# Optimization experiments

Measured on AMD Instinct MI355X. Metric: run time of the kernel, lower is better.

Reference implementation:

```python
import jax, jax.numpy as jnp
import numpy as np

N_NODES = 200000  # graph size
D = 128           # feature dim == out_size
N1 = 81920        # layer-1 node set size
B = 8192          # batch size
K = 10            # num_sample neighbors


def setup_inputs() -> dict:
    key = jax.random.key(0)
    k = jax.random.split(key, 7)
    raw_features = jax.random.normal(k[0], (N_NODES, D), dtype=jnp.float32)
    # xavier-like scale for weights [out, 2*in]
    W1 = jax.random.normal(k[1], (D, 2 * D), dtype=jnp.float32) * (1.0 / np.sqrt(2 * D))
    W2 = jax.random.normal(k[2], (D, 2 * D), dtype=jnp.float32) * (1.0 / np.sqrt(2 * D))
    layer1_nodes = jax.random.randint(k[3], (N1,), 0, N_NODES)
    neigh0_idx = jax.random.randint(k[4], (N1, K), 0, N_NODES)
    map_batch = jax.random.randint(k[5], (B,), 0, N1)
    neigh1_idx = jax.random.randint(k[6], (B, K), 0, N1)
    return {
        "raw_features": raw_features,
        "W1": W1,
        "W2": W2,
        "layer1_nodes": layer1_nodes,
        "neigh0_idx": neigh0_idx,
        "map_batch": map_batch,
        "neigh1_idx": neigh1_idx,
    }


def _sage_layer(self_feats, agg_feats, W):
    # combined = cat([self, agg], dim=1); relu(W @ combined.T).T == relu(combined @ W.T)
    combined = jnp.concatenate([self_feats, agg_feats], axis=1)
    return jax.nn.relu(combined @ W.T)


def reference(raw_features, W1, W2, layer1_nodes, neigh0_idx, map_batch, neigh1_idx):
    # Layer 1: aggregate raw features over K sampled neighbors (MEAN), gcn=False
    agg0 = jnp.mean(raw_features[neigh0_idx], axis=1)        # [N1, D]
    self0 = raw_features[layer1_nodes]                        # [N1, D]
    h1 = _sage_layer(self0, agg0, W1)                         # [N1, D]
    # Layer 2: aggregate layer-1 embeddings for the batch nodes
    agg1 = jnp.mean(h1[neigh1_idx], axis=1)                   # [B, D]
    self1 = h1[map_batch]                                     # [B, D]
    h2 = _sage_layer(self1, agg1, W2)                         # [B, D]
    return h2
```

## Files before the change

### kernel.cpp

```cpp
#include <hip/hip_runtime.h>
#include <stdint.h>

#define D 128
#define K_NEI 10
#define TILE_M 64

typedef __bf16 bf16x8 __attribute__((ext_vector_type(8)));
typedef float f32x4 __attribute__((ext_vector_type(4)));

__device__ __forceinline__ uint32_t f2bf(float f) {
    union { float f; uint32_t u; } v; v.f = f;
    uint32_t u = v.u;
    return (u + 0x7FFFu + ((u >> 16) & 1u)) >> 16;
}
__device__ __forceinline__ float bf2f(uint32_t h) {
    union { uint32_t u; float f; } v; v.u = h << 16; return v.f;
}
__device__ __forceinline__ uint32_t pack2(float a, float b) {
    return f2bf(a) | (f2bf(b) << 16);
}

__global__ void convert_W(const float* __restrict__ W, uint16_t* __restrict__ Wb)
{
    int t = blockIdx.x * 256 + threadIdx.x;
    int c = t >> 4, j = t & 15;
    const float* src = W + (size_t)(c & 127) * 256 + (c >> 7) * 128 + j * 8;
    f32x4 a = *(const f32x4*)src;
    f32x4 b = *(const f32x4*)(src + 4);
    uint4 o;
    o.x = pack2(a[0], a[1]); o.y = pack2(a[2], a[3]);
    o.z = pack2(b[0], b[1]); o.w = pack2(b[2], b[3]);
    *(uint4*)(Wb + (size_t)c * 128 + j * 8) = o;
}

template <bool A_F32>
__global__ void gemm_P(const void* __restrict__ Asrc_,
                       const uint16_t* __restrict__ Wb,
                       uint16_t* __restrict__ P)
{
    __shared__ __align__(16) uint16_t Alds[TILE_M * 128];
    __shared__ __align__(16) uint16_t Wlds[128 * 128];

    const int tid  = threadIdx.x;
    const int wave = tid >> 6;
    const int lane = tid & 63;
    const int r16  = lane & 15;
    const int q    = lane >> 4;
    const int G    = blockIdx.x * TILE_M;

    #pragma unroll
    for (int it = 0; it < 4; ++it) {
        int t = it * 256 + tid;
        int n = t >> 4, c = t & 15;
        uint4 o;
        if (A_F32) {
            const float* src = (const float*)Asrc_ + (size_t)(G + n) * D + c * 8;
            f32x4 a = *(const f32x4*)src;
            f32x4 b = *(const f32x4*)(src + 4);
            o.x = pack2(a[0], a[1]); o.y = pack2(a[2], a[3]);
            o.z = pack2(b[0], b[1]); o.w = pack2(b[2], b[3]);
        } else {
            o = *(const uint4*)((const uint16_t*)Asrc_ + (size_t)(G + n) * D + c * 8);
        }
        int cs = c ^ (n & 15);
        *(uint4*)(Alds + n * 128 + cs * 8) = o;
    }

    f32x4 acc[2][8];
    #pragma unroll
    for (int h = 0; h < 2; ++h)
        #pragma unroll
        for (int nt = 0; nt < 8; ++nt) acc[h][nt] = (f32x4){0.f, 0.f, 0.f, 0.f};

    for (int h = 0; h < 2; ++h) {
        #pragma unroll
        for (int it = 0; it < 8; ++it) {
            int t = it * 256 + tid;
            int j = t >> 4, c = t & 15;
            uint4 v = *(const uint4*)(Wb + (size_t)(h * 128 + j) * 128 + c * 8);
            int cs = c ^ (j & 15);
            *(uint4*)(Wlds + j * 128 + cs * 8) = v;
        }
        __syncthreads();

        #pragma unroll
        for (int ks = 0; ks < 4; ++ks) {
            int cidx = ks * 4 + q;
            bf16x8 a = *(const bf16x8*)(Alds + (wave * 16 + r16) * 128 + ((cidx ^ r16) * 8));
            bf16x8 b[8];
            #pragma unroll
            for (int nt = 0; nt < 8; ++nt) {
                int jj = nt * 16 + r16;
                b[nt] = *(const bf16x8*)(Wlds + jj * 128 + ((cidx ^ r16) * 8));
            }
            #pragma unroll
            for (int nt = 0; nt < 8; ++nt)
                acc[h][nt] = __builtin_amdgcn_mfma_f32_16x16x32_bf16(a, b[nt], acc[h][nt], 0, 0, 0);
        }
        __syncthreads();
    }

    const int row_base = G + wave * 16 + q * 4;
    #pragma unroll
    for (int h = 0; h < 2; ++h)
        #pragma unroll
        for (int nt = 0; nt < 8; ++nt) {
            int col = h * 128 + nt * 16 + r16;
            #pragma unroll
            for (int r = 0; r < 4; ++r)
                P[(size_t)(row_base + r) * 256 + col] = (uint16_t)f2bf(acc[h][nt][r]);
        }
}

template <bool OUT_F32>
__global__ void combine(const uint16_t* __restrict__ P,
                        const int* __restrict__ self_idx,
                        const int* __restrict__ neigh_idx,
                        void* __restrict__ out_, int M)
{
    const int t = blockIdx.x * 256 + threadIdx.x;
    const int i = t >> 4;
    const int j = t & 15;
    if (i >= M) return;

    uint4 sv = *(const uint4*)(P + (size_t)self_idx[i] * 256 + j * 8);

    const int* nrow = neigh_idx + (size_t)i * K_NEI;
    int idx[K_NEI];
    #pragma unroll
    for (int k = 0; k < K_NEI; ++k) idx[k] = nrow[k];

    float s0=0,s1=0,s2=0,s3=0,s4=0,s5=0,s6=0,s7=0;
    #pragma unroll
    for (int k = 0; k < K_NEI; ++k) {
        uint4 v = *(const uint4*)(P + (size_t)idx[k] * 256 + 128 + j * 8);
        s0 += bf2f(v.x & 0xFFFFu); s1 += bf2f(v.x >> 16);
        s2 += bf2f(v.y & 0xFFFFu); s3 += bf2f(v.y >> 16);
        s4 += bf2f(v.z & 0xFFFFu); s5 += bf2f(v.z >> 16);
        s6 += bf2f(v.w & 0xFFFFu); s7 += bf2f(v.w >> 16);
    }
    const float inv = 0.1f;
    float r0 = bf2f(sv.x & 0xFFFFu) + s0 * inv, r1 = bf2f(sv.x >> 16) + s1 * inv;
    float r2 = bf2f(sv.y & 0xFFFFu) + s2 * inv, r3 = bf2f(sv.y >> 16) + s3 * inv;
    float r4 = bf2f(sv.z & 0xFFFFu) + s4 * inv, r5 = bf2f(sv.z >> 16) + s5 * inv;
    float r6 = bf2f(sv.w & 0xFFFFu) + s6 * inv, r7 = bf2f(sv.w >> 16) + s7 * inv;
    r0 = r0 > 0.f ? r0 : 0.f; r1 = r1 > 0.f ? r1 : 0.f;
    r2 = r2 > 0.f ? r2 : 0.f; r3 = r3 > 0.f ? r3 : 0.f;
    r4 = r4 > 0.f ? r4 : 0.f; r5 = r5 > 0.f ? r5 : 0.f;
    r6 = r6 > 0.f ? r6 : 0.f; r7 = r7 > 0.f ? r7 : 0.f;

    if (OUT_F32) {
        float* dst = (float*)out_ + (size_t)i * D + j * 8;
        *(f32x4*)dst       = (f32x4){r0, r1, r2, r3};
        *(f32x4*)(dst + 4) = (f32x4){r4, r5, r6, r7};
    } else {
        uint4 o;
        o.x = pack2(r0, r1); o.y = pack2(r2, r3);
        o.z = pack2(r4, r5); o.w = pack2(r6, r7);
        *(uint4*)((uint16_t*)out_ + (size_t)i * D + j * 8) = o;
    }
}

template <bool FEATS_F32>
__global__ void build_A(const void* __restrict__ feats_,
                        const int* __restrict__ self_idx,
                        const int* __restrict__ neigh_idx,
                        uint16_t* __restrict__ A, int M)
{
    const int t = blockIdx.x * 256 + threadIdx.x;
    const int i = t >> 4;
    const int j = t & 15;
    if (i >= M) return;

    const float*    ff = (const float*)feats_;
    const uint16_t* fb = (const uint16_t*)feats_;

    {
        int node = self_idx[i];
        uint4 o;
        if (FEATS_F32) {
            const float* src = ff + (size_t)node * D + j * 8;
            f32x4 a = *(const f32x4*)src;
            f32x4 b = *(const f32x4*)(src + 4);
            o.x = pack2(a[0], a[1]); o.y = pack2(a[2], a[3]);
            o.z = pack2(b[0], b[1]); o.w = pack2(b[2], b[3]);
        } else {
            o = *(const uint4*)(fb + (size_t)node * D + j * 8);
        }
        *(uint4*)(A + (size_t)i * 256 + j * 8) = o;
    }

    const int* nrow = neigh_idx + (size_t)i * K_NEI;
    int idx[K_NEI];
    #pragma unroll
    for (int k = 0; k < K_NEI; ++k) idx[k] = nrow[k];

    float s0=0,s1=0,s2=0,s3=0,s4=0,s5=0,s6=0,s7=0;
    #pragma unroll
    for (int k = 0; k < K_NEI; ++k) {
        if (FEATS_F32) {
            const float* src = ff + (size_t)idx[k] * D + j * 8;
            f32x4 a = *(const f32x4*)src;
            f32x4 b = *(const f32x4*)(src + 4);
            s0 += a[0]; s1 += a[1]; s2 += a[2]; s3 += a[3];
            s4 += b[0]; s5 += b[1]; s6 += b[2]; s7 += b[3];
        } else {
            uint4 v = *(const uint4*)(fb + (size_t)idx[k] * D + j * 8);
            s0 += bf2f(v.x & 0xFFFFu); s1 += bf2f(v.x >> 16);
            s2 += bf2f(v.y & 0xFFFFu); s3 += bf2f(v.y >> 16);
            s4 += bf2f(v.z & 0xFFFFu); s5 += bf2f(v.z >> 16);
            s6 += bf2f(v.w & 0xFFFFu); s7 += bf2f(v.w >> 16);
        }
    }
    const float inv = 0.1f;
    uint4 o;
    o.x = pack2(s0 * inv, s1 * inv);
    o.y = pack2(s2 * inv, s3 * inv);
    o.z = pack2(s4 * inv, s5 * inv);
    o.w = pack2(s6 * inv, s7 * inv);
    *(uint4*)(A + (size_t)i * 256 + 128 + j * 8) = o;
}

template <bool OUT_F32>
__global__ void gemm_relu(const uint16_t* __restrict__ A,
                          const float* __restrict__ W,
                          void* __restrict__ out_)
{
    __shared__ __align__(16) uint16_t Alds[TILE_M * 128];
    __shared__ __align__(16) uint16_t Wlds[128 * 128];

    const int tid  = threadIdx.x;
    const int wave = tid >> 6;
    const int lane = tid & 63;
    const int r16  = lane & 15;
    const int q    = lane >> 4;
    const int G    = blockIdx.x * TILE_M;

    f32x4 acc[8];
    #pragma unroll
    for (int nt = 0; nt < 8; ++nt) acc[nt] = (f32x4){0.f, 0.f, 0.f, 0.f};

    for (int half = 0; half < 2; ++half) {
        #pragma unroll
        for (int it = 0; it < 8; ++it) {
            int t = it * 256 + tid;
            int j = t >> 4, c = t & 15;
            const float* src = W + (size_t)j * 256 + half * 128 + c * 8;
            f32x4 w0 = *(const f32x4*)(src);
            f32x4 w1 = *(const f32x4*)(src + 4);
            uint4 o;
            o.x = pack2(w0[0], w0[1]); o.y = pack2(w0[2], w0[3]);
            o.z = pack2(w1[0], w1[1]); o.w = pack2(w1[2], w1[3]);
            int cs = c ^ (j & 15);
            *(uint4*)(Wlds + j * 128 + cs * 8) = o;
        }
        #pragma unroll
        for (int it = 0; it < 4; ++it) {
            int t = it * 256 + tid;
            int n = t >> 4, c = t & 15;
            uint4 v = *(const uint4*)(A + (size_t)(G + n) * 256 + half * 128 + c * 8);
            int cs = c ^ (n & 15);
            *(uint4*)(Alds + n * 128 + cs * 8) = v;
        }
        __syncthreads();

        #pragma unroll
        for (int ks = 0; ks < 4; ++ks) {
            int cidx = ks * 4 + q;
            bf16x8 a = *(const bf16x8*)(Alds + (wave * 16 + r16) * 128 + ((cidx ^ r16) * 8));
            bf16x8 b[8];
            #pragma unroll
            for (int nt = 0; nt < 8; ++nt) {
                int jj = nt * 16 + r16;
                b[nt] = *(const bf16x8*)(Wlds + jj * 128 + ((cidx ^ r16) * 8));
            }
            #pragma unroll
            for (int nt = 0; nt < 8; ++nt)
                acc[nt] = __builtin_amdgcn_mfma_f32_16x16x32_bf16(a, b[nt], acc[nt], 0, 0, 0);
        }
        __syncthreads();
    }

    const int row_base = G + wave * 16 + q * 4;
    #pragma unroll
    for (int nt = 0; nt < 8; ++nt) {
        int col = nt * 16 + r16;
        #pragma unroll
        for (int r = 0; r < 4; ++r) {
            float v = acc[nt][r];
            v = v > 0.f ? v : 0.f;
            if (OUT_F32) ((float*)out_)[(size_t)(row_base + r) * D + col] = v;
            else ((uint16_t*)out_)[(size_t)(row_base + r) * D + col] = (uint16_t)f2bf(v);
        }
    }
}

extern "C" void kernel_launch(void* const* d_in, const int* in_sizes, int n_in,
                              void* d_out, int out_size, void* d_ws, size_t ws_size,
                              hipStream_t stream) {
    const float* raw = (const float*)d_in[0];
    const float* W1  = (const float*)d_in[1];
    const float* W2  = (const float*)d_in[2];
    const int* layer1_nodes = (const int*)d_in[3];
    const int* neigh0       = (const int*)d_in[4];
    const int* map_batch    = (const int*)d_in[5];
    const int* neigh1       = (const int*)d_in[6];

    const int N_NODES = in_sizes[0] / D;
    const int N1 = in_sizes[3];
    const int B  = in_sizes[5];

    const size_t szP  = (size_t)N_NODES * 256 * 2;
    const size_t szQ  = (size_t)N1 * 256 * 2;
    const size_t szH1 = (size_t)N1 * 128 * 2;
    const size_t szW  = 256 * 128 * 2;
    const size_t needA = (szP > szQ ? szP : szQ) + szH1 + 2 * szW;

    if (ws_size >= needA && (N_NODES % TILE_M) == 0 && (N1 % TILE_M) == 0) {
        uint16_t* Pbuf = (uint16_t*)d_ws;
        uint16_t* h1   = (uint16_t*)((char*)d_ws + (szP > szQ ? szP : szQ));
        uint16_t* W1b  = h1 + (size_t)N1 * 128;
        uint16_t* W2b  = W1b + 256 * 128;

        convert_W<<<16, 256, 0, stream>>>(W1, W1b);
        convert_W<<<16, 256, 0, stream>>>(W2, W2b);
        gemm_P<true ><<<N_NODES / TILE_M, 256, 0, stream>>>(raw, W1b, Pbuf);
        combine<false><<<(N1 * 16 + 255) / 256, 256, 0, stream>>>(Pbuf, layer1_nodes, neigh0, h1, N1);
        gemm_P<false><<<N1 / TILE_M, 256, 0, stream>>>(h1, W2b, Pbuf);
        combine<true ><<<(B * 16 + 255) / 256, 256, 0, stream>>>(Pbuf, map_batch, neigh1, d_out, B);
        return;
    }

    const size_t needB = (size_t)N1 * 256 * 2 + (size_t)N1 * 128 * 2 + (size_t)B * 256 * 2;
    if (ws_size >= needB) {
        uint16_t* A1 = (uint16_t*)d_ws;
        uint16_t* h1 = A1 + (size_t)N1 * 256;
        uint16_t* A2 = h1 + (size_t)N1 * 128;

        build_A<true ><<<(N1 * 16 + 255) / 256, 256, 0, stream>>>(raw, layer1_nodes, neigh0, A1, N1);
        gemm_relu<false><<<N1 / TILE_M, 256, 0, stream>>>(A1, W1, h1);
        build_A<false><<<(B * 16 + 255) / 256, 256, 0, stream>>>(h1, map_batch, neigh1, A2, B);
        gemm_relu<true ><<<B / TILE_M, 256, 0, stream>>>(A2, W2, d_out);
    }
}
```

Before: 244.6 us.

## Make projection GEMM persistent with resident weights and register prefetch

The per-tile projection GEMM becomes a persistent kernel. It loads the full 256x128 bf16 weight matrix into shared memory once per block, then has each wave loop over 16-row tiles, reading A straight into registers and prefetching the next tile. This removes the repeated weight staging and the A shared-memory round trip that happened for every 64-row tile. The two weight conversions are merged into one launch, and neighbor indices are loaded as int2. The fallback path is replaced by a fused gather+GEMM layer kernel. The trade-off is 64KB of shared memory per block, which lowers occupancy.

```diff
diff --git a/kernel.cpp b/kernel.cpp
--- a/kernel.cpp
+++ b/kernel.cpp
@@ -19,10 +19,16 @@
 __device__ __forceinline__ uint32_t pack2(float a, float b) {
     return f2bf(a) | (f2bf(b) << 16);
 }
-
-__global__ void convert_W(const float* __restrict__ W, uint16_t* __restrict__ Wb)
+__device__ __forceinline__ bf16x8 u4_as_bf16x8(uint4 u) {
+    union { uint4 u; bf16x8 b; } v; v.u = u; return v.b;
+}
+
+__global__ void convert_W2(const float* __restrict__ Wa, const float* __restrict__ Wb_in,
+                           uint16_t* __restrict__ Oa, uint16_t* __restrict__ Ob)
 {
-    int t = blockIdx.x * 256 + threadIdx.x;
+    const float* W = (blockIdx.x < 16) ? Wa : Wb_in;
+    uint16_t*    O = (blockIdx.x < 16) ? Oa : Ob;
+    int t = (blockIdx.x & 15) * 256 + threadIdx.x;
     int c = t >> 4, j = t & 15;
     const float* src = W + (size_t)(c & 127) * 256 + (c >> 7) * 128 + j * 8;
     f32x4 a = *(const f32x4*)src;
@@ -30,86 +36,121 @@
     uint4 o;
     o.x = pack2(a[0], a[1]); o.y = pack2(a[2], a[3]);
     o.z = pack2(b[0], b[1]); o.w = pack2(b[2], b[3]);
-    *(uint4*)(Wb + (size_t)c * 128 + j * 8) = o;
+    *(uint4*)(O + (size_t)c * 128 + j * 8) = o;
 }
 
 template <bool A_F32>
-__global__ void gemm_P(const void* __restrict__ Asrc_,
-                       const uint16_t* __restrict__ Wb,
-                       uint16_t* __restrict__ P)
+__global__ __launch_bounds__(256)
+void gemm_ws(const void* __restrict__ Asrc_,
+             const uint16_t* __restrict__ Wb,
+             uint16_t* __restrict__ P, int M)
 {
-    __shared__ __align__(16) uint16_t Alds[TILE_M * 128];
-    __shared__ __align__(16) uint16_t Wlds[128 * 128];
+    __shared__ __align__(16) uint16_t Wlds[256 * 128];
 
     const int tid  = threadIdx.x;
     const int wave = tid >> 6;
     const int lane = tid & 63;
     const int r16  = lane & 15;
     const int q    = lane >> 4;
-    const int G    = blockIdx.x * TILE_M;
-
-    #pragma unroll
-    for (int it = 0; it < 4; ++it) {
+
+    #pragma unroll
+    for (int it = 0; it < 16; ++it) {
         int t = it * 256 + tid;
-        int n = t >> 4, c = t & 15;
-        uint4 o;
+        int j = t >> 4, c = t & 15;
+        uint4 v = *(const uint4*)(Wb + (size_t)j * 128 + c * 8);
+        int cs = c ^ (j & 15);
+        *(uint4*)(Wlds + j * 128 + cs * 8) = v;
+    }
+    __syncthreads();
+
+    const int nTiles = M >> 4;
+    const int stride = gridDim.x * 4;
+    int tile = blockIdx.x * 4 + wave;
+    if (tile >= nTiles) return;
+
+    f32x4 preF[8];  uint4 preB[4];
+
+    if (A_F32) {
+        const float* row = (const float*)Asrc_ + (size_t)(tile * 16 + r16) * D + q * 8;
+        #pragma unroll
+        for (int ks = 0; ks < 4; ++ks) {
+            preF[2 * ks]     = *(const f32x4*)(row + ks * 32);
+            preF[2 * ks + 1] = *(const f32x4*)(row + ks * 32 + 4);
+        }
+    } else {
+        const uint16_t* row = (const uint16_t*)Asrc_ + (size_t)(tile * 16 + r16) * D + q * 8;
+        #pragma unroll
+        for (int ks = 0; ks < 4; ++ks)
+            preB[ks] = *(const uint4*)(row + ks * 32);
+    }
+
+    while (tile < nTiles) {
+        const int nxt = tile + stride;
+
+        bf16x8 a[4];
         if (A_F32) {
-            const float* src = (const float*)Asrc_ + (size_t)(G + n) * D + c * 8;
-            f32x4 a = *(const f32x4*)src;
-            f32x4 b = *(const f32x4*)(src + 4);
-            o.x = pack2(a[0], a[1]); o.y = pack2(a[2], a[3]);
-            o.z = pack2(b[0], b[1]); o.w = pack2(b[2], b[3]);
+            #pragma unroll
+            for (int ks = 0; ks < 4; ++ks) {
+                uint4 u;
+                u.x = pack2(preF[2*ks][0],   preF[2*ks][1]);
+                u.y = pack2(preF[2*ks][2],   preF[2*ks][3]);
+                u.z = pack2(preF[2*ks+1][0], preF[2*ks+1][1]);
+                u.w = pack2(preF[2*ks+1][2], preF[2*ks+1][3]);
+                a[ks] = u4_as_bf16x8(u);
+            }
         } else {
-            o = *(const uint4*)((const uint16_t*)Asrc_ + (size_t)(G + n) * D + c * 8);
-        }
-        int cs = c ^ (n & 15);
-        *(uint4*)(Alds + n * 128 + cs * 8) = o;
-    }
-
-    f32x4 acc[2][8];
-    #pragma unroll
-    for (int h = 0; h < 2; ++h)
-        #pragma unroll
-        for (int nt = 0; nt < 8; ++nt) acc[h][nt] = (f32x4){0.f, 0.f, 0.f, 0.f};
-
-    for (int h = 0; h < 2; ++h) {
-        #pragma unroll
-        for (int it = 0; it < 8; ++it) {
-            int t = it * 256 + tid;
-            int j = t >> 4, c = t & 15;
-            uint4 v = *(const uint4*)(Wb + (size_t)(h * 128 + j) * 128 + c * 8);
-            int cs = c ^ (j & 15);
-            *(uint4*)(Wlds + j * 128 + cs * 8) = v;
-        }
-        __syncthreads();
-
-        #pragma unroll
-        for (int ks = 0; ks < 4; ++ks) {
-            int cidx = ks * 4 + q;
-            bf16x8 a = *(const bf16x8*)(Alds + (wave * 16 + r16) * 128 + ((cidx ^ r16) * 8));
-            bf16x8 b[8];
+            #pragma unroll
+            for (int ks = 0; ks < 4; ++ks) a[ks] = u4_as_bf16x8(preB[ks]);
+        }
+
+        if (nxt < nTiles) {
+            if (A_F32) {
+                const float* row = (const float*)Asrc_ + (size_t)(nxt * 16 + r16) * D + q * 8;
+                #pragma unroll
+                for (int ks = 0; ks < 4; ++ks) {
+                    preF[2 * ks]     = *(const f32x4*)(row + ks * 32);
+                    preF[2 * ks + 1] = *(const f32x4*)(row + ks * 32 + 4);
+                }
+            } else {
+                const uint16_t* row = (const uint16_t*)Asrc_ + (size_t)(nxt * 16 + r16) * D + q * 8;
+                #pragma unroll
+                for (int ks = 0; ks < 4; ++ks)
+                    preB[ks] = *(const uint4*)(row + ks * 32);
+            }
+        }
+
+        f32x4 acc[2][8];
+        #pragma unroll
+        for (int h = 0; h < 2; ++h)
+            #pragma unroll
+            for (int nt = 0; nt < 8; ++nt) acc[h][nt] = (f32x4){0.f, 0.f, 0.f, 0.f};
+
+        #pragma unroll
+        for (int h = 0; h < 2; ++h)
+            #pragma unroll
+            for (int ks = 0; ks < 4; ++ks) {
+                const int cidx = ks * 4 + q;
+                #pragma unroll
+                for (int nt = 0; nt < 8; ++nt) {
+                    const int jj = h * 128 + nt * 16 + r16;
+                    bf16x8 b = *(const bf16x8*)(Wlds + jj * 128 + ((cidx ^ r16) * 8));
+                    acc[h][nt] = __builtin_amdgcn_mfma_f32_16x16x32_bf16(a[ks], b, acc[h][nt], 0, 0, 0);
+                }
+            }
+
+        const int row0 = tile * 16 + q * 4;
+        #pragma unroll
+        for (int h = 0; h < 2; ++h)
             #pragma unroll
             for (int nt = 0; nt < 8; ++nt) {
-                int jj = nt * 16 + r16;
-                b[nt] = *(const bf16x8*)(Wlds + jj * 128 + ((cidx ^ r16) * 8));
-            }
-            #pragma unroll
-            for (int nt = 0; nt < 8; ++nt)
-                acc[h][nt] = __builtin_amdgcn_mfma_f32_16x16x32_bf16(a, b[nt], acc[h][nt], 0, 0, 0);
-        }
-        __syncthreads();
-    }
-
-    const int row_base = G + wave * 16 + q * 4;
-    #pragma unroll
-    for (int h = 0; h < 2; ++h)
-        #pragma unroll
-        for (int nt = 0; nt < 8; ++nt) {
-            int col = h * 128 + nt * 16 + r16;
-            #pragma unroll
-            for (int r = 0; r < 4; ++r)
-                P[(size_t)(row_base + r) * 256 + col] = (uint16_t)f2bf(acc[h][nt][r]);
-        }
+                const int col = h * 128 + nt * 16 + r16;
+                #pragma unroll
+                for (int r = 0; r < 4; ++r)
+                    P[(size_t)(row0 + r) * 256 + col] = (uint16_t)f2bf(acc[h][nt][r]);
+            }
+
+        tile = nxt;
+    }
 }
 
 template <bool OUT_F32>
@@ -125,10 +166,13 @@
 
     uint4 sv = *(const uint4*)(P + (size_t)self_idx[i] * 256 + j * 8);
 
-    const int* nrow = neigh_idx + (size_t)i * K_NEI;
+    const int2* nrow2 = (const int2*)(neigh_idx + (size_t)i * K_NEI);
     int idx[K_NEI];
     #pragma unroll
-    for (int k = 0; k < K_NEI; ++k) idx[k] = nrow[k];
+    for (int k = 0; k < 5; ++k) {
+        int2 p = nrow2[k];
+        idx[2 * k] = p.x; idx[2 * k + 1] = p.y;
+    }
 
     float s0=0,s1=0,s2=0,s3=0,s4=0,s5=0,s6=0,s7=0;
     #pragma unroll
@@ -161,70 +205,12 @@
     }
 }
 
-template <bool FEATS_F32>
-__global__ void build_A(const void* __restrict__ feats_,
-                        const int* __restrict__ self_idx,
-                        const int* __restrict__ neigh_idx,
-                        uint16_t* __restrict__ A, int M)
-{
-    const int t = blockIdx.x * 256 + threadIdx.x;
-    const int i = t >> 4;
-    const int j = t & 15;
-    if (i >= M) return;
-
-    const float*    ff = (const float*)feats_;
-    const uint16_t* fb = (const uint16_t*)feats_;
-
-    {
-        int node = self_idx[i];
-        uint4 o;
-        if (FEATS_F32) {
-            const float* src = ff + (size_t)node * D + j * 8;
-            f32x4 a = *(const f32x4*)src;
-            f32x4 b = *(const f32x4*)(src + 4);
-            o.x = pack2(a[0], a[1]); o.y = pack2(a[2], a[3]);
-            o.z = pack2(b[0], b[1]); o.w = pack2(b[2], b[3]);
-        } else {
-            o = *(const uint4*)(fb + (size_t)node * D + j * 8);
-        }
-        *(uint4*)(A + (size_t)i * 256 + j * 8) = o;
-    }
-
-    const int* nrow = neigh_idx + (size_t)i * K_NEI;
-    int idx[K_NEI];
-    #pragma unroll
-    for (int k = 0; k < K_NEI; ++k) idx[k] = nrow[k];
-
-    float s0=0,s1=0,s2=0,s3=0,s4=0,s5=0,s6=0,s7=0;
-    #pragma unroll
-    for (int k = 0; k < K_NEI; ++k) {
-        if (FEATS_F32) {
-            const float* src = ff + (size_t)idx[k] * D + j * 8;
-            f32x4 a = *(const f32x4*)src;
-            f32x4 b = *(const f32x4*)(src + 4);
-            s0 += a[0]; s1 += a[1]; s2 += a[2]; s3 += a[3];
-            s4 += b[0]; s5 += b[1]; s6 += b[2]; s7 += b[3];
-        } else {
-            uint4 v = *(const uint4*)(fb + (size_t)idx[k] * D + j * 8);
-            s0 += bf2f(v.x & 0xFFFFu); s1 += bf2f(v.x >> 16);
-            s2 += bf2f(v.y & 0xFFFFu); s3 += bf2f(v.y >> 16);
-            s4 += bf2f(v.z & 0xFFFFu); s5 += bf2f(v.z >> 16);
-            s6 += bf2f(v.w & 0xFFFFu); s7 += bf2f(v.w >> 16);
-        }
-    }
-    const float inv = 0.1f;
-    uint4 o;
-    o.x = pack2(s0 * inv, s1 * inv);
-    o.y = pack2(s2 * inv, s3 * inv);
-    o.z = pack2(s4 * inv, s5 * inv);
-    o.w = pack2(s6 * inv, s7 * inv);
-    *(uint4*)(A + (size_t)i * 256 + 128 + j * 8) = o;
-}
-
-template <bool OUT_F32>
-__global__ void gemm_relu(const uint16_t* __restrict__ A,
-                          const float* __restrict__ W,
-                          void* __restrict__ out_)
+template <bool FEATS_F32, bool OUT_F32>
+__global__ void sage_layer(const void* __restrict__ feats_,
+                           const float* __restrict__ W,
+                           const int* __restrict__ self_idx,
+                           const int* __restrict__ neigh_idx,
+                           void* __restrict__ out_)
 {
     __shared__ __align__(16) uint16_t Alds[TILE_M * 128];
     __shared__ __align__(16) uint16_t Wlds[128 * 128];
@@ -235,6 +221,9 @@
     const int r16  = lane & 15;
     const int q    = lane >> 4;
     const int G    = blockIdx.x * TILE_M;
+
+    const float*    feats_f = (const float*)feats_;
+    const uint16_t* feats_b = (const uint16_t*)feats_;
 
     f32x4 acc[8];
     #pragma unroll
@@ -254,13 +243,57 @@
             int cs = c ^ (j & 15);
             *(uint4*)(Wlds + j * 128 + cs * 8) = o;
         }
-        #pragma unroll
-        for (int it = 0; it < 4; ++it) {
-            int t = it * 256 + tid;
-            int n = t >> 4, c = t & 15;
-            uint4 v = *(const uint4*)(A + (size_t)(G + n) * 256 + half * 128 + c * 8);
-            int cs = c ^ (n & 15);
-            *(uint4*)(Alds + n * 128 + cs * 8) = v;
+        if (half == 0) {
+            #pragma unroll
+            for (int it = 0; it < 4; ++it) {
+                int t = it * 256 + tid;
+                int n = t >> 4, c = t & 15;
+                int node = self_idx[G + n];
+                uint4 o;
+                if (FEATS_F32) {
+                    const float* src = feats_f + (size_t)node * D + c * 8;
+                    f32x4 f0 = *(const f32x4*)(src);
+                    f32x4 f1 = *(const f32x4*)(src + 4);
+                    o.x = pack2(f0[0], f0[1]); o.y = pack2(f0[2], f0[3]);
+                    o.z = pack2(f1[0], f1[1]); o.w = pack2(f1[2], f1[3]);
+                } else {
+                    o = *(const uint4*)(feats_b + (size_t)node * D + c * 8);
+                }
+                int cs = c ^ (n & 15);
+                *(uint4*)(Alds + n * 128 + cs * 8) = o;
+            }
+        } else {
+            #pragma unroll
+            for (int it = 0; it < 4; ++it) {
+                int t = it * 256 + tid;
+                int n = t >> 4, c = t & 15;
+                const int* nrow = neigh_idx + (size_t)(G + n) * K_NEI;
+                float s0=0,s1=0,s2=0,s3=0,s4=0,s5=0,s6=0,s7=0;
+                #pragma unroll
+                for (int k = 0; k < K_NEI; ++k) {
+                    if (FEATS_F32) {
+                        const float* src = feats_f + (size_t)nrow[k] * D + c * 8;
+                        f32x4 f0 = *(const f32x4*)(src);
+                        f32x4 f1 = *(const f32x4*)(src + 4);
+                        s0 += f0[0]; s1 += f0[1]; s2 += f0[2]; s3 += f0[3];
+                        s4 += f1[0]; s5 += f1[1]; s6 += f1[2]; s7 += f1[3];
+                    } else {
+                        uint4 v = *(const uint4*)(feats_b + (size_t)nrow[k] * D + c * 8);
+                        s0 += bf2f(v.x & 0xFFFFu); s1 += bf2f(v.x >> 16);
+                        s2 += bf2f(v.y & 0xFFFFu); s3 += bf2f(v.y >> 16);
+                        s4 += bf2f(v.z & 0xFFFFu); s5 += bf2f(v.z >> 16);
+                        s6 += bf2f(v.w & 0xFFFFu); s7 += bf2f(v.w >> 16);
+                    }
+                }
+                const float inv = 0.1f;
+                uint4 o;
+                o.x = pack2(s0 * inv, s1 * inv);
+                o.y = pack2(s2 * inv, s3 * inv);
+                o.z = pack2(s4 * inv, s5 * inv);
+                o.w = pack2(s6 * inv, s7 * inv);
+                int cs = c ^ (n & 15);
+                *(uint4*)(Alds + n * 128 + cs * 8) = o;
+            }
         }
         __syncthreads();
 
@@ -316,30 +349,30 @@
     const size_t szW  = 256 * 128 * 2;
     const size_t needA = (szP > szQ ? szP : szQ) + szH1 + 2 * szW;
 
-    if (ws_size >= needA && (N_NODES % TILE_M) == 0 && (N1 % TILE_M) == 0) {
+    if (ws_size >= needA && (N_NODES % 16) == 0 && (N1 % 16) == 0 && (B % 16) == 0) {
         uint16_t* Pbuf = (uint16_t*)d_ws;
         uint16_t* h1   = (uint16_t*)((char*)d_ws + (szP > szQ ? szP : szQ));
         uint16_t* W1b  = h1 + (size_t)N1 * 128;
         uint16_t* W2b  = W1b + 256 * 128;
 
-        convert_W<<<16, 256, 0, stream>>>(W1, W1b);
-        convert_W<<<16, 256, 0, stream>>>(W2, W2b);
-        gemm_P<true ><<<N_NODES / TILE_M, 256, 0, stream>>>(raw, W1b, Pbuf);
+        convert_W2<<<32, 256, 0, stream>>>(W1, W2, W1b, W2b);
+
+        int tiles1 = N_NODES >> 4;
+        int grid1  = 1024;
+        gemm_ws<true ><<<grid1, 256, 0, stream>>>(raw, W1b, Pbuf, N_NODES);
+
         combine<false><<<(N1 * 16 + 255) / 256, 256, 0, stream>>>(Pbuf, layer1_nodes, neigh0, h1, N1);
-        gemm_P<false><<<N1 / TILE_M, 256, 0, stream>>>(h1, W2b, Pbuf);
+
+        int tiles2 = N1 >> 4;
+        int grid2  = (tiles2 + 3) / 4;
+        if (grid2 > 1280) grid2 = 1280;
+        gemm_ws<false><<<grid2, 256, 0, stream>>>(h1, W2b, Pbuf, N1);
+
         combine<true ><<<(B * 16 + 255) / 256, 256, 0, stream>>>(Pbuf, map_batch, neigh1, d_out, B);
         return;
     }
 
-    const size_t needB = (size_t)N1 * 256 * 2 + (size_t)N1 * 128 * 2 + (size_t)B * 256 * 2;
-    if (ws_size >= needB) {
-        uint16_t* A1 = (uint16_t*)d_ws;
-        uint16_t* h1 = A1 + (size_t)N1 * 256;
-        uint16_t* A2 = h1 + (size_t)N1 * 128;
-
-        build_A<true ><<<(N1 * 16 + 255) / 256, 256, 0, stream>>>(raw, layer1_nodes, neigh0, A1, N1);
-        gemm_relu<false><<<N1 / TILE_M, 256, 0, stream>>>(A1, W1, h1);
-        build_A<false><<<(B * 16 + 255) / 256, 256, 0, stream>>>(h1, map_batch, neigh1, A2, B);
-        gemm_relu<true ><<<B / TILE_M, 256, 0, stream>>>(A2, W2, d_out);
-    }
-}
+    uint16_t* h1 = (uint16_t*)d_ws;
+    sage_layer<true,  false><<<N1 / TILE_M, 256, 0, stream>>>(raw, W1, layer1_nodes, neigh0, h1);
+    sage_layer<false, true ><<<B  / TILE_M, 256, 0, stream>>>(h1,  W2, map_batch,    neigh1, d_out);
+}
```

Result: no change. 243.2 us (-0.5%).
